# Optimization experiments

Measured on AMD Instinct MI355X. Metric: run time of the kernel, lower is better.

## Reference

```python
import jax, jax.numpy as jnp
import numpy as np

C, H, W, P = 3, 32, 32, 16
Z = P * P  # 256
B, S = 128, 1024
EPS = 1e-06
MAX_VAL, MIN_VAL = 5.0, -5.0


def setup_inputs() -> dict:
    key = jax.random.key(0)
    ks = jax.random.split(key, 8)
    patches = jax.random.normal(ks[0], (B, S, Z), dtype=jnp.float32)
    pos_channels = jax.random.randint(ks[1], (B, S), 0, C)
    pos_h = jax.random.randint(ks[2], (B, S), 0, H)
    pos_w = jax.random.randint(ks[3], (B, S), 0, W)
    key_pad_mask = jax.random.randint(ks[4], (B, S), 0, 2).astype(bool)
    # running Welford stats buffers (simulate partially-trained state)
    n = 100.0 * jax.random.uniform(ks[5], (C, H, W), dtype=jnp.float32)
    mean = jax.random.normal(ks[6], (C, H, W, Z), dtype=jnp.float32)
    m2 = 10.0 * jax.random.uniform(ks[7], (C, H, W, Z), dtype=jnp.float32)
    return {"patches": patches, "pos_channels": pos_channels, "pos_h": pos_h,
            "pos_w": pos_w, "key_pad_mask": key_pad_mask, "n": n, "mean": mean, "m2": m2}


def _patchnorm(patches, pos_channels, pos_h, pos_w, key_pad_mask, n, mean, m2):
    # Flatten token dims; padded tokens are masked (contribute 0) instead of
    # boolean-compressed, keeping shapes static under jit.
    N = B * S
    p = patches.reshape(N, Z)
    valid = (~key_pad_mask).reshape(N).astype(p.dtype)  # [N]
    flat = (pos_channels * (H * W) + pos_h * W + pos_w).reshape(N)  # [N]

    n_flat = n.reshape(C * H * W)
    mean_flat = mean.reshape(C * H * W, Z)
    m2_flat = m2.reshape(C * H * W, Z)

    # --- Welford batched update (matches torch scatter_add_3d sequence) ---
    n_new = n_flat.at[flat].add(valid)                         # n += 1 per valid token
    delta = p - mean_flat[flat]                                # gather old mean
    contrib = (delta * valid[:, None]) / jnp.maximum(n_new[flat], 1.0)[:, None]
    mean_new = mean_flat.at[flat].add(contrib)                 # mean += delta/n
    delta2 = p - mean_new[flat]                                # gather new mean
    m2_new = m2_flat.at[flat].add(delta * delta2 * valid[:, None])

    # --- variance / std (var=1 where n<2) ---
    var = m2_new / jnp.maximum(n_new, 1.0)[:, None]
    var = jnp.where((n_new < 2.0)[:, None], 1.0, var)
    std = jnp.sqrt(var)

    # --- normalize with updated stats, clamp, zero out padding ---
    normed = (p - mean_new[flat]) / (std[flat] + EPS)
    normed = jnp.clip(normed, MIN_VAL, MAX_VAL) * valid[:, None]
    return normed.reshape(B, S, Z)


def reference(patches, pos_channels, pos_h, pos_w, key_pad_mask, n, mean, m2):
    return _patchnorm(patches, pos_channels, pos_h, pos_w, key_pad_mask, n, mean, m2)
```

## Files before the change

kernel.cpp:

```cpp
#include <hip/hip_runtime.h>

#define HH 32
#define WW 32
#define NCELL 3072
#define NTOK  (128*1024)
#define CAP   128
#define EPSV  1e-6f

typedef float v4f __attribute__((ext_vector_type(4)));


__global__ __launch_bounds__(256) void zero_kernel(int* __restrict__ cnt) {
    cnt[blockIdx.x * 256 + threadIdx.x] = 0;
}

__global__ __launch_bounds__(256) void build_kernel(
        const int* __restrict__ pc, const int* __restrict__ ph,
        const int* __restrict__ pw, const int* __restrict__ mask,
        int* __restrict__ cnt, int* __restrict__ list) {
    int t = blockIdx.x * 256 + threadIdx.x;
    int cell = pc[t] * (HH * WW) + ph[t] * WW + pw[t];
    int valid = (mask[t] == 0);
    int r = atomicAdd(&cnt[cell], valid ? 1 : 0x10000);
    int slot = valid ? (r & 0xFFFF) : (CAP - 1 - (r >> 16));
    if (slot >= 0 && slot < CAP) list[cell * CAP + slot] = t;
}

__global__ __launch_bounds__(256, 8) void cell_kernel(
        const v4f* __restrict__ patch4, const float* __restrict__ nbuf,
        const v4f* __restrict__ mean4,  const v4f* __restrict__ m24,
        const int* __restrict__ cnt_,   const int* __restrict__ list,
        v4f* __restrict__ out4) {
    __shared__ int slist[CAP];
    __shared__ v4f part_sq[256];
    __shared__ v4f part_ss[256];
    const int c    = blockIdx.x;
    const int tid  = threadIdx.x;
    const int wave = tid >> 6;
    const int lane = tid & 63;

    if (tid < CAP) slist[tid] = list[c * CAP + tid];
    int cw = cnt_[c];
    int vcnt = cw & 0xFFFF;
    int icnt = cw >> 16;
    if (vcnt > CAP) vcnt = CAP;
    if (icnt > CAP - vcnt) icnt = CAP - vcnt;
    __syncthreads();

    for (int i = wave; i < icnt; i += 4) {
        int t = slist[CAP - 1 - i];
        __builtin_nontemporal_store((v4f)0.0f, &out4[t * 64 + lane]);
    }

    const float n_new = nbuf[c] + (float)vcnt;
    const float denom = fmaxf(n_new, 1.0f);
    const v4f   m_old = mean4[c * 64 + lane];

    v4f sq = (v4f)0.0f, ss = (v4f)0.0f;
    #pragma unroll 4
    for (int i = wave; i < vcnt; i += 4) {
        int t = slist[i];
        v4f p = patch4[t * 64 + lane];
        v4f q = p - m_old;
        sq += q;
        ss += q * q;
    }
    part_sq[tid] = sq;
    part_ss[tid] = ss;
    __syncthreads();

    const v4f Sq = part_sq[lane] + part_sq[64 + lane] +
                   part_sq[128 + lane] + part_sq[192 + lane];
    const v4f Ss = part_ss[lane] + part_ss[64 + lane] +
                   part_ss[128 + lane] + part_ss[192 + lane];

    const v4f m2v = m24[c * 64 + lane];
    const v4f dm  = Sq / denom;
    const v4f mn  = m_old + dm;
    v4f var = (m2v + (Ss - dm * Sq)) / denom;
    if (n_new < 2.0f) var = (v4f)1.0f;
    v4f inv;
    inv.x = 1.0f / (sqrtf(var.x) + EPSV);
    inv.y = 1.0f / (sqrtf(var.y) + EPSV);
    inv.z = 1.0f / (sqrtf(var.z) + EPSV);
    inv.w = 1.0f / (sqrtf(var.w) + EPSV);

    #pragma unroll 2
    for (int i = wave; i < vcnt; i += 4) {
        int t = slist[i];
        v4f p = patch4[t * 64 + lane];
        v4f u = (p - mn) * inv;
        v4f o;
        o.x = fminf(fmaxf(u.x, -5.0f), 5.0f);
        o.y = fminf(fmaxf(u.y, -5.0f), 5.0f);
        o.z = fminf(fmaxf(u.z, -5.0f), 5.0f);
        o.w = fminf(fmaxf(u.w, -5.0f), 5.0f);
        __builtin_nontemporal_store(o, &out4[t * 64 + lane]);
    }
}

extern "C" void kernel_launch(void* const* d_in, const int* in_sizes, int n_in,
                              void* d_out, int out_size, void* d_ws, size_t ws_size,
                              hipStream_t stream) {
    const float* patches = (const float*)d_in[0];
    const int*   pc      = (const int*)  d_in[1];
    const int*   ph      = (const int*)  d_in[2];
    const int*   pw      = (const int*)  d_in[3];
    const int*   mask    = (const int*)  d_in[4];
    const float* nbuf    = (const float*)d_in[5];
    const float* mean    = (const float*)d_in[6];
    const float* m2      = (const float*)d_in[7];
    float*       out     = (float*)d_out;

    int* cnt  = (int*)d_ws;
    int* list = cnt + NCELL;

    zero_kernel <<<NCELL / 256, 256, 0, stream>>>(cnt);
    build_kernel<<<NTOK / 256,  256, 0, stream>>>(pc, ph, pw, mask, cnt, list);

    cell_kernel<<<NCELL, 256, 0, stream>>>(
        (const v4f*)patches, nbuf, (const v4f*)mean, (const v4f*)m2,
        cnt, list, (v4f*)out);
}
```

Measured before the change: 262.1 us.

## Split per-cell stats pass from streaming per-token normalize kernel

Splits the fused cell kernel in two. The first kernel computes only the per-cell mean and inverse std into a workspace buffer. A second grid-stride kernel then walks tokens in order, gathers the stats and writes normalized output, zeros included. This turns scattered per-cell writes into sequential streaming writes and balances load across blocks, at the cost of reading patches twice from memory plus one extra launch and a stats round-trip. Patch loads are also marked nontemporal.

```diff
diff --git a/kernel.cpp b/kernel.cpp
--- a/kernel.cpp
+++ b/kernel.cpp
@@ -6,6 +6,7 @@
 #define NTOK  (128*1024)
 #define CAP   128
 #define EPSV  1e-6f
+#define NBLK  4096
 
 typedef float v4f __attribute__((ext_vector_type(4)));
 
@@ -22,15 +23,17 @@
     int cell = pc[t] * (HH * WW) + ph[t] * WW + pw[t];
     int valid = (mask[t] == 0);
     int r = atomicAdd(&cnt[cell], valid ? 1 : 0x10000);
-    int slot = valid ? (r & 0xFFFF) : (CAP - 1 - (r >> 16));
-    if (slot >= 0 && slot < CAP) list[cell * CAP + slot] = t;
+    if (valid) {
+        int slot = r & 0xFFFF;
+        if (slot < CAP) list[cell * CAP + slot] = t;
+    }
 }
 
-__global__ __launch_bounds__(256, 8) void cell_kernel(
+__global__ __launch_bounds__(256, 8) void stats_kernel(
         const v4f* __restrict__ patch4, const float* __restrict__ nbuf,
         const v4f* __restrict__ mean4,  const v4f* __restrict__ m24,
         const int* __restrict__ cnt_,   const int* __restrict__ list,
-        v4f* __restrict__ out4) {
+        v4f* __restrict__ stats4) {
     __shared__ int slist[CAP];
     __shared__ v4f part_sq[256];
     __shared__ v4f part_ss[256];
@@ -40,27 +43,16 @@
     const int lane = tid & 63;
 
     if (tid < CAP) slist[tid] = list[c * CAP + tid];
-    int cw = cnt_[c];
-    int vcnt = cw & 0xFFFF;
-    int icnt = cw >> 16;
+    int vcnt = cnt_[c] & 0xFFFF;
     if (vcnt > CAP) vcnt = CAP;
-    if (icnt > CAP - vcnt) icnt = CAP - vcnt;
     __syncthreads();
 
-    for (int i = wave; i < icnt; i += 4) {
-        int t = slist[CAP - 1 - i];
-        __builtin_nontemporal_store((v4f)0.0f, &out4[t * 64 + lane]);
-    }
-
-    const float n_new = nbuf[c] + (float)vcnt;
-    const float denom = fmaxf(n_new, 1.0f);
-    const v4f   m_old = mean4[c * 64 + lane];
-
+    const v4f m_old = mean4[c * 64 + lane];
     v4f sq = (v4f)0.0f, ss = (v4f)0.0f;
     #pragma unroll 4
     for (int i = wave; i < vcnt; i += 4) {
         int t = slist[i];
-        v4f p = patch4[t * 64 + lane];
+        v4f p = __builtin_nontemporal_load(&patch4[t * 64 + lane]);
         v4f q = p - m_old;
         sq += q;
         ss += q * q;
@@ -69,32 +61,49 @@
     part_ss[tid] = ss;
     __syncthreads();
 
-    const v4f Sq = part_sq[lane] + part_sq[64 + lane] +
-                   part_sq[128 + lane] + part_sq[192 + lane];
-    const v4f Ss = part_ss[lane] + part_ss[64 + lane] +
-                   part_ss[128 + lane] + part_ss[192 + lane];
+    if (tid < 64) {
+        const v4f Sq = part_sq[lane] + part_sq[64 + lane] +
+                       part_sq[128 + lane] + part_sq[192 + lane];
+        const v4f Ss = part_ss[lane] + part_ss[64 + lane] +
+                       part_ss[128 + lane] + part_ss[192 + lane];
+        const float n_new = nbuf[c] + (float)vcnt;
+        const float denom = fmaxf(n_new, 1.0f);
+        const v4f m2v = m24[c * 64 + lane];
+        const v4f dm  = Sq / denom;
+        const v4f mn  = m_old + dm;
+        v4f var = (m2v + (Ss - dm * Sq)) / denom;
+        if (n_new < 2.0f) var = (v4f)1.0f;
+        v4f inv;
+        inv.x = 1.0f / (sqrtf(var.x) + EPSV);
+        inv.y = 1.0f / (sqrtf(var.y) + EPSV);
+        inv.z = 1.0f / (sqrtf(var.z) + EPSV);
+        inv.w = 1.0f / (sqrtf(var.w) + EPSV);
+        stats4[c * 128 + lane * 2]     = mn;
+        stats4[c * 128 + lane * 2 + 1] = inv;
+    }
+}
 
-    const v4f m2v = m24[c * 64 + lane];
-    const v4f dm  = Sq / denom;
-    const v4f mn  = m_old + dm;
-    v4f var = (m2v + (Ss - dm * Sq)) / denom;
-    if (n_new < 2.0f) var = (v4f)1.0f;
-    v4f inv;
-    inv.x = 1.0f / (sqrtf(var.x) + EPSV);
-    inv.y = 1.0f / (sqrtf(var.y) + EPSV);
-    inv.z = 1.0f / (sqrtf(var.z) + EPSV);
-    inv.w = 1.0f / (sqrtf(var.w) + EPSV);
-
-    #pragma unroll 2
-    for (int i = wave; i < vcnt; i += 4) {
-        int t = slist[i];
-        v4f p = patch4[t * 64 + lane];
-        v4f u = (p - mn) * inv;
-        v4f o;
-        o.x = fminf(fmaxf(u.x, -5.0f), 5.0f);
-        o.y = fminf(fmaxf(u.y, -5.0f), 5.0f);
-        o.z = fminf(fmaxf(u.z, -5.0f), 5.0f);
-        o.w = fminf(fmaxf(u.w, -5.0f), 5.0f);
+__global__ __launch_bounds__(256, 8) void norm_kernel(
+        const v4f* __restrict__ patch4, const int* __restrict__ pc,
+        const int* __restrict__ ph,     const int* __restrict__ pw,
+        const int* __restrict__ mask,   const v4f* __restrict__ stats4,
+        v4f* __restrict__ out4) {
+    const int tid  = threadIdx.x;
+    const int wave = tid >> 6;
+    const int lane = tid & 63;
+    for (int t = blockIdx.x * 4 + wave; t < NTOK; t += NBLK * 4) {
+        v4f o = (v4f)0.0f;
+        if (mask[t] == 0) {
+            int cell = pc[t] * (HH * WW) + ph[t] * WW + pw[t];
+            v4f p   = __builtin_nontemporal_load(&patch4[t * 64 + lane]);
+            v4f mn  = stats4[cell * 128 + lane * 2];
+            v4f inv = stats4[cell * 128 + lane * 2 + 1];
+            v4f u = (p - mn) * inv;
+            o.x = fminf(fmaxf(u.x, -5.0f), 5.0f);
+            o.y = fminf(fmaxf(u.y, -5.0f), 5.0f);
+            o.z = fminf(fmaxf(u.z, -5.0f), 5.0f);
+            o.w = fminf(fmaxf(u.w, -5.0f), 5.0f);
+        }
         __builtin_nontemporal_store(o, &out4[t * 64 + lane]);
     }
 }
@@ -112,13 +121,17 @@
     const float* m2      = (const float*)d_in[7];
     float*       out     = (float*)d_out;
 
-    int* cnt  = (int*)d_ws;
-    int* list = cnt + NCELL;
+    int* cnt    = (int*)d_ws;
+    int* list   = cnt + NCELL;
+    v4f* stats4 = (v4f*)(list + NCELL * CAP);
 
     zero_kernel <<<NCELL / 256, 256, 0, stream>>>(cnt);
     build_kernel<<<NTOK / 256,  256, 0, stream>>>(pc, ph, pw, mask, cnt, list);
 
-    cell_kernel<<<NCELL, 256, 0, stream>>>(
+    stats_kernel<<<NCELL, 256, 0, stream>>>(
         (const v4f*)patches, nbuf, (const v4f*)mean, (const v4f*)m2,
-        cnt, list, (v4f*)out);
+        cnt, list, stats4);
+
+    norm_kernel<<<NBLK, 256, 0, stream>>>(
+        (const v4f*)patches, pc, ph, pw, mask, stats4, (v4f*)out);
 }
```

Result: slower. 270.9 us (+3.3%).
